# Optimization experiments

Measured on AMD Instinct MI355X. Metric: run time of the kernel, lower is better.

The kernel has to match this reference:

```python
import jax, jax.numpy as jnp
import numpy as np

IMG = 2048
STRIDES = [8, 16, 32, 64, 128]
A = 9                       # num_cell_anchors
CLASS_NUM = 16              # num_classes - 1
TOPK = 1000                 # config.test_layer_topk
MAX_DELTA = float(np.log(1000.0 / 16.0))

_LEVEL_N = [(IMG // s) * (IMG // s) * A for s in STRIDES]


def setup_inputs() -> dict:
    key = jax.random.key(0)
    inp = {}
    for l, n in enumerate(_LEVEL_N):
        key, k1, k2, k3, k4 = jax.random.split(key, 5)
        cxcy = jax.random.uniform(k1, (n, 2), minval=0.0, maxval=float(IMG))
        wh = jax.random.uniform(k2, (n, 2), minval=8.0, maxval=128.0)
        inp[f"anchors{l}"] = jnp.concatenate([cxcy - 0.5 * wh, cxcy + 0.5 * wh], axis=1)
        # logits biased negative like a trained RetinaNet cls head (prior_prob init)
        inp[f"cls{l}"] = jax.random.normal(k3, (1, n, CLASS_NUM), dtype=jnp.float32) - 4.0
        inp[f"reg{l}"] = jax.random.normal(k4, (1, n, 8), dtype=jnp.float32) * 0.1
    return inp


def bbox_transform_inv(rois, deltas):
    # standard box decode (restore_bbox with unnormalize=False)
    w = rois[:, 2] - rois[:, 0]
    h = rois[:, 3] - rois[:, 1]
    cx = rois[:, 0] + 0.5 * w
    cy = rois[:, 1] + 0.5 * h
    pcx = cx + deltas[:, 0] * w
    pcy = cy + deltas[:, 1] * h
    pw = w * jnp.exp(jnp.minimum(deltas[:, 2], MAX_DELTA))
    ph = h * jnp.exp(jnp.minimum(deltas[:, 3], MAX_DELTA))
    return jnp.stack([pcx - 0.5 * pw, pcy - 0.5 * ph,
                      pcx + 0.5 * pw, pcy + 0.5 * ph], axis=1)


def _per_layer(anchors, pred_cls, pred_reg):
    a = anchors.reshape(-1, 4)
    c = pred_cls[0].reshape(-1, CLASS_NUM)
    r = pred_reg[0].reshape(-1, 8)[:, :4]
    if a.shape[0] > TOPK:
        ruler = jnp.max(c, axis=1)                  # max score over classes
        _, inds = jax.lax.top_k(ruler, TOPK)        # irregular topk + gather
        a = jnp.take(a, inds, axis=0)
        c = jnp.take(c, inds, axis=0)
        r = jnp.take(r, inds, axis=0)
    return a, jax.nn.sigmoid(c), r


def reference(anchors0, cls0, reg0, anchors1, cls1, reg1, anchors2, cls2, reg2,
              anchors3, cls3, reg3, anchors4, cls4, reg4):
    levels = [(anchors0, cls0, reg0), (anchors1, cls1, reg1),
              (anchors2, cls2, reg2), (anchors3, cls3, reg3),
              (anchors4, cls4, reg4)]
    kept = [_per_layer(a, c, r) for a, c, r in levels]
    keep_anchors = jnp.concatenate([k[0] for k in kept], axis=0)   # [K,4]
    keep_cls = jnp.concatenate([k[1] for k in kept], axis=0)       # [K,C]
    keep_reg = jnp.concatenate([k[2] for k in kept], axis=0)       # [K,4]
    K = keep_cls.shape[0]
    tag = jnp.tile(jnp.arange(CLASS_NUM, dtype=keep_cls.dtype) + 1.0, (K,)).reshape(-1, 1)
    pred_scores = keep_cls.reshape(-1, 1)                          # [K*C,1]
    pred_bbox = bbox_transform_inv(keep_anchors, keep_reg)         # [K,4]
    pred_bbox = jnp.tile(pred_bbox, (1, CLASS_NUM)).reshape(-1, 4) # [K*C,4]
    return jnp.concatenate([pred_bbox, pred_scores, tag], axis=1)  # [K*C,6]
```

## Files before the change

kernel.cpp:

```cpp
#include <hip/hip_runtime.h>
#include <math.h>

#define NLEV 5
#define TOPKK 1000
#define NCLS 16
#define NPART 16
#define HP 4
#define PART_CAP 256
#define CAND_TOT 2048
#define NCHUNK 3069u
#define CPB 6u
#define NB 512u
#define HISTSZ (NLEV * 256)

__device__ __forceinline__ int lev_of_chunk(unsigned c) {
    if (c < 2304u) return 0;
    if (c < 2880u) return 1;
    if (c < 3024u) return 2;
    if (c < 3060u) return 3;
    return 4;
}
__device__ __forceinline__ unsigned lev_base(int l) {
    unsigned b = 0u;
    if (l == 1) b = 589824u;
    if (l == 2) b = 737280u;
    if (l == 3) b = 774144u;
    if (l == 4) b = 783360u;
    return b;
}

struct Ptrs {
    const float* anc[NLEV];
    const float* cls[NLEV];
    const float* reg[NLEV];
};

__device__ __forceinline__ unsigned f2key(float f) {
    unsigned u = __float_as_uint(f);
    return (u & 0x80000000u) ? ~u : (u | 0x80000000u);
}

__device__ __forceinline__ float max4(float4 v) {
    return fmaxf(fmaxf(v.x, v.y), fmaxf(v.z, v.w));
}

__device__ __forceinline__ void arrive_wait(unsigned* base, bool dowait) {
    __syncthreads();
    if (threadIdx.x == 0) {
        __builtin_amdgcn_fence(__ATOMIC_RELEASE, "agent");
        unsigned g = blockIdx.x & 15u;
        unsigned a = __hip_atomic_fetch_add(base + g * 16u, 1u,
                        __ATOMIC_RELAXED, __HIP_MEMORY_SCOPE_AGENT);
        if (a == NB / 16u - 1u) {
            unsigned m = __hip_atomic_fetch_add(base + 256u, 1u,
                            __ATOMIC_RELAXED, __HIP_MEMORY_SCOPE_AGENT);
            if (m == 15u) {
                #pragma unroll
                for (unsigned r = 0; r < 16u; r++)
                    __hip_atomic_store(base + 512u + r * 16u, 1u,
                                       __ATOMIC_RELAXED, __HIP_MEMORY_SCOPE_AGENT);
            }
        }
        if (dowait) {
            while (!__hip_atomic_load(base + 512u + g * 16u,
                        __ATOMIC_RELAXED, __HIP_MEMORY_SCOPE_AGENT))
                __builtin_amdgcn_s_sleep(4);
            __builtin_amdgcn_fence(__ATOMIC_ACQUIRE, "agent");
        }
    }
    __syncthreads();
}

__device__ __forceinline__ void sel256(unsigned c, unsigned rem,
                                       unsigned* wsum, unsigned* aux) {
    int t = threadIdx.x, lane = t & 63, wv = t >> 6;
    unsigned s = c;
    #pragma unroll
    for (int d = 1; d < 64; d <<= 1) {
        unsigned o = __shfl_down(s, d, 64);
        if (lane + d < 64) s += o;
    }
    if (lane == 0) wsum[wv] = s;
    __syncthreads();
    unsigned incl = s;
    #pragma unroll
    for (int w2 = 1; w2 < 4; w2++) if (wv + w2 < 4) incl += wsum[wv + w2];
    unsigned above = incl - c;
    if (above < rem && rem <= incl) {
        aux[0] = (unsigned)t;
        aux[1] = rem - above;
    }
    __syncthreads();
}

__global__ __launch_bounds__(256, 2) void k_fused(Ptrs p, unsigned* histA,
        unsigned* histB, unsigned* cnt, unsigned* bar,
        unsigned long long* cand, float* out) {
    __shared__ unsigned long long lbuf[CAND_TOT];
    __shared__ unsigned hh[256];
    __shared__ unsigned wsum[4];
    __shared__ unsigned aux[33];

    const unsigned b = blockIdx.x;
    const int t = threadIdx.x;
    const unsigned c0 = b * CPB;
    const int lev = lev_of_chunk(c0);
    const unsigned ebase = lev_base(lev);

    unsigned keys[CPB];
    hh[t] = 0u;
    __syncthreads();
    #pragma unroll
    for (unsigned j = 0; j < CPB; j++) {
        unsigned ch = c0 + j;
        unsigned k = 0u;
        if (ch < NCHUNK) {
            unsigned loc = ch * 256u + (unsigned)t - ebase;
            const float4* cp = (const float4*)(p.cls[lev]) + (size_t)loc * 4;
            float4 v0 = cp[0], v1 = cp[1], v2 = cp[2], v3 = cp[3];
            float m = fmaxf(fmaxf(max4(v0), max4(v1)), fmaxf(max4(v2), max4(v3)));
            k = f2key(m);
            atomicAdd(&hh[k >> 24], 1u);
        }
        keys[j] = k;
    }
    __syncthreads();
    {
        unsigned v = hh[t];
        if (v) atomicAdd(&histA[(b & (HP - 1u)) * HISTSZ
                                + (unsigned)lev * 256u + (unsigned)t], v);
    }
    arrive_wait(bar, true);

    unsigned cA = 0;
    #pragma unroll
    for (int pp = 0; pp < HP; pp++) cA += histA[pp * HISTSZ + lev * 256 + t];
    sel256(cA, TOPKK, wsum, aux);
    unsigned binA = aux[0], remA = aux[1];
    __syncthreads();

    hh[t] = 0u;
    __syncthreads();
    #pragma unroll
    for (unsigned j = 0; j < CPB; j++) {
        unsigned k = keys[j];
        if ((c0 + j) < NCHUNK && (k >> 24) == binA)
            atomicAdd(&hh[(k >> 16) & 0xFFu], 1u);
    }
    __syncthreads();
    {
        unsigned v = hh[t];
        if (v) atomicAdd(&histB[(b & (HP - 1u)) * HISTSZ
                                + (unsigned)lev * 256u + (unsigned)t], v);
    }
    arrive_wait(bar + 1024, true);

    unsigned cB = 0;
    #pragma unroll
    for (int pp = 0; pp < HP; pp++) cB += histB[pp * HISTSZ + lev * 256 + t];
    sel256(cB, remA, wsum, aux);
    unsigned thresh = (binA << 24) | (aux[0] << 16);
    __syncthreads();

    #pragma unroll
    for (unsigned j = 0; j < CPB; j++) {
        unsigned ch = c0 + j;
        unsigned k = keys[j];
        if (ch < NCHUNK && k >= thresh) {
            unsigned loc = ch * 256u + (unsigned)t - ebase;
            unsigned part = ch & (NPART - 1u);
            unsigned slot = atomicAdd(&cnt[lev * NPART + part], 1u);
            if (slot < PART_CAP)
                cand[((size_t)(lev * NPART + part)) * PART_CAP + slot] =
                    ((unsigned long long)k << 32) | (unsigned)(~loc);
        }
    }

    bool ranker = b < (unsigned)(NLEV * 8);
    arrive_wait(bar + 2048, ranker);
    if (!ranker) return;

    const float MAXD = 4.135166556742356f;
    int l = (int)(b >> 3);
    unsigned sl = b & 7u;

    if (t < NPART) {
        unsigned cc = cnt[l * NPART + t];
        aux[t] = (cc > PART_CAP) ? PART_CAP : cc;
    }
    __syncthreads();
    if (t == 0) {
        unsigned o = 0;
        for (int pp = 0; pp < NPART; pp++) { aux[16 + pp] = o; o += aux[pp]; }
        aux[32] = (o > CAND_TOT) ? CAND_TOT : o;
    }
    __syncthreads();
    unsigned n = aux[32];
    for (int pp = 0; pp < NPART; pp++) {
        unsigned cc = aux[pp], o = aux[16 + pp];
        for (unsigned e = (unsigned)t; e < cc; e += 256u) {
            unsigned dst = o + e;
            if (dst < CAND_TOT)
                lbuf[dst] = cand[((size_t)(l * NPART + pp)) * PART_CAP + e];
        }
    }
    __syncthreads();

    unsigned j = sl * 256u + (unsigned)t;
    if (j >= n) return;
    unsigned long long my = lbuf[j];
    unsigned rank = 0;
    #pragma unroll 8
    for (unsigned q = 0; q < n; q++) rank += (lbuf[q] > my) ? 1u : 0u;
    if (rank >= TOPKK) return;

    unsigned idx = ~((unsigned)(my & 0xFFFFFFFFull));
    float4 an = ((const float4*)p.anc[l])[idx];
    float4 dd = ((const float4*)p.reg[l])[(size_t)idx * 2];
    float w = an.z - an.x, h = an.w - an.y;
    float cx = an.x + 0.5f * w, cy = an.y + 0.5f * h;
    float pcx = cx + dd.x * w, pcy = cy + dd.y * h;
    float pw = w * expf(fminf(dd.z, MAXD));
    float ph = h * expf(fminf(dd.w, MAXD));
    float bx = pcx - 0.5f * pw, by = pcy - 0.5f * ph;
    float bz = pcx + 0.5f * pw, bw = pcy + 0.5f * ph;

    const float4* cp = (const float4*)(p.cls[l]) + (size_t)idx * 4;
    float sg[16];
    #pragma unroll
    for (int g = 0; g < 4; g++) {
        float4 v = cp[g];
        sg[4 * g + 0] = 1.0f / (1.0f + expf(-v.x));
        sg[4 * g + 1] = 1.0f / (1.0f + expf(-v.y));
        sg[4 * g + 2] = 1.0f / (1.0f + expf(-v.z));
        sg[4 * g + 3] = 1.0f / (1.0f + expf(-v.w));
    }
    float4* q = (float4*)(out + (size_t)(l * TOPKK + rank) * (NCLS * 6));
    #pragma unroll
    for (int g = 0; g < 8; g++) {
        float ta = (float)(2 * g + 1), tb = (float)(2 * g + 2);
        q[3 * g + 0] = make_float4(bx, by, bz, bw);
        q[3 * g + 1] = make_float4(sg[2 * g], ta, bx, by);
        q[3 * g + 2] = make_float4(bz, bw, sg[2 * g + 1], tb);
    }
}

extern "C" void kernel_launch(void* const* d_in, const int* in_sizes, int n_in,
                              void* d_out, int out_size, void* d_ws, size_t ws_size,
                              hipStream_t stream) {
    (void)in_sizes; (void)n_in; (void)out_size; (void)ws_size;
    Ptrs p;
    for (int l = 0; l < NLEV; l++) {
        p.anc[l] = (const float*)d_in[3 * l + 0];
        p.cls[l] = (const float*)d_in[3 * l + 1];
        p.reg[l] = (const float*)d_in[3 * l + 2];
    }

    char* w = (char*)d_ws;
    unsigned* histA = (unsigned*)w;
    unsigned* histB = (unsigned*)(w + 20480);
    unsigned* cnt   = (unsigned*)(w + 40960);
    unsigned* bar   = (unsigned*)(w + 41280);
    unsigned long long* cand = (unsigned long long*)(w + 53568);
    float* out = (float*)d_out;

    (void)hipMemsetAsync(w, 0, 53568, stream);
    k_fused<<<dim3(NB), dim3(256), 0, stream>>>(p, histA, histB, cnt, bar,
                                                cand, out);
}
```

Before: 202.0 us.

## Replace counter grid barrier with flag-array monitor barrier and spread atomic contention

The grid barrier changes from hierarchical atomic counters to per-block arrival flags. Block 0 polls all 512 flags with its 256 threads and then releases 16 go-flags. Global histogram atomics are spread over 16 partitions instead of 4, and the candidate partition counters are padded onto separate cache lines, both to cut atomic contention. In exchange the workspace memset grows, the post-barrier histogram reads go from 4 to 16 partitions, and all blocks must wait on block 0 polling serially.

```diff
diff --git a/kernel.cpp b/kernel.cpp
--- a/kernel.cpp
+++ b/kernel.cpp
@@ -5,13 +5,14 @@
 #define TOPKK 1000
 #define NCLS 16
 #define NPART 16
-#define HP 4
+#define HP 16u
 #define PART_CAP 256
 #define CAND_TOT 2048
 #define NCHUNK 3069u
 #define CPB 6u
 #define NB 512u
 #define HISTSZ (NLEV * 256)
+#define BAR_STRIDE 1024u
 
 __device__ __forceinline__ int lev_of_chunk(unsigned c) {
     if (c < 2304u) return 0;
@@ -44,29 +45,51 @@
     return fmaxf(fmaxf(v.x, v.y), fmaxf(v.z, v.w));
 }
 
-__device__ __forceinline__ void arrive_wait(unsigned* base, bool dowait) {
-    __syncthreads();
+__device__ __forceinline__ void bar_arrive(unsigned* inst) {
     if (threadIdx.x == 0) {
         __builtin_amdgcn_fence(__ATOMIC_RELEASE, "agent");
-        unsigned g = blockIdx.x & 15u;
-        unsigned a = __hip_atomic_fetch_add(base + g * 16u, 1u,
+        __hip_atomic_store(inst + blockIdx.x, 1u, __ATOMIC_RELAXED,
+                           __HIP_MEMORY_SCOPE_AGENT);
+    }
+}
+
+__device__ __forceinline__ void bar_monitor_fanout(unsigned* inst, unsigned* wsh) {
+    for (;;) {
+        unsigned f0 = __hip_atomic_load(inst + (unsigned)threadIdx.x,
                         __ATOMIC_RELAXED, __HIP_MEMORY_SCOPE_AGENT);
-        if (a == NB / 16u - 1u) {
-            unsigned m = __hip_atomic_fetch_add(base + 256u, 1u,
-                            __ATOMIC_RELAXED, __HIP_MEMORY_SCOPE_AGENT);
-            if (m == 15u) {
-                #pragma unroll
-                for (unsigned r = 0; r < 16u; r++)
-                    __hip_atomic_store(base + 512u + r * 16u, 1u,
-                                       __ATOMIC_RELAXED, __HIP_MEMORY_SCOPE_AGENT);
-            }
-        }
-        if (dowait) {
-            while (!__hip_atomic_load(base + 512u + g * 16u,
-                        __ATOMIC_RELAXED, __HIP_MEMORY_SCOPE_AGENT))
-                __builtin_amdgcn_s_sleep(4);
+        unsigned f1 = __hip_atomic_load(inst + 256u + (unsigned)threadIdx.x,
+                        __ATOMIC_RELAXED, __HIP_MEMORY_SCOPE_AGENT);
+        unsigned long long bal = __ballot(f0 != 0u && f1 != 0u);
+        if ((threadIdx.x & 63) == 0)
+            wsh[threadIdx.x >> 6] = (bal == 0xFFFFFFFFFFFFFFFFull) ? 1u : 0u;
+        __syncthreads();
+        bool done = wsh[0] && wsh[1] && wsh[2] && wsh[3];
+        __syncthreads();
+        if (done) break;
+        __builtin_amdgcn_s_sleep(2);
+    }
+    if (threadIdx.x < 16)
+        __hip_atomic_store(inst + 768u + (unsigned)threadIdx.x * 16u, 1u,
+                           __ATOMIC_RELAXED, __HIP_MEMORY_SCOPE_AGENT);
+}
+
+__device__ __forceinline__ void bar_waitgo(unsigned* inst) {
+    unsigned g = blockIdx.x & 15u;
+    while (!__hip_atomic_load(inst + 768u + g * 16u, __ATOMIC_RELAXED,
+                              __HIP_MEMORY_SCOPE_AGENT))
+        __builtin_amdgcn_s_sleep(4);
+    __builtin_amdgcn_fence(__ATOMIC_ACQUIRE, "agent");
+}
+
+__device__ __forceinline__ void gridbar(unsigned* inst, unsigned* wsh) {
+    __syncthreads();
+    bar_arrive(inst);
+    if (blockIdx.x == 0) {
+        bar_monitor_fanout(inst, wsh);
+        if (threadIdx.x == 0)
             __builtin_amdgcn_fence(__ATOMIC_ACQUIRE, "agent");
-        }
+    } else if (threadIdx.x == 0) {
+        bar_waitgo(inst);
     }
     __syncthreads();
 }
@@ -99,6 +122,7 @@
     __shared__ unsigned long long lbuf[CAND_TOT];
     __shared__ unsigned hh[256];
     __shared__ unsigned wsum[4];
+    __shared__ unsigned wsh[4];
     __shared__ unsigned aux[33];
 
     const unsigned b = blockIdx.x;
@@ -106,10 +130,11 @@
     const unsigned c0 = b * CPB;
     const int lev = lev_of_chunk(c0);
     const unsigned ebase = lev_base(lev);
+    unsigned* bar0 = bar;
+    unsigned* bar1 = bar + BAR_STRIDE;
+    unsigned* bar2 = bar + 2u * BAR_STRIDE;
 
     unsigned keys[CPB];
-    hh[t] = 0u;
-    __syncthreads();
     #pragma unroll
     for (unsigned j = 0; j < CPB; j++) {
         unsigned ch = c0 + j;
@@ -120,21 +145,25 @@
             float4 v0 = cp[0], v1 = cp[1], v2 = cp[2], v3 = cp[3];
             float m = fmaxf(fmaxf(max4(v0), max4(v1)), fmaxf(max4(v2), max4(v3)));
             k = f2key(m);
-            atomicAdd(&hh[k >> 24], 1u);
         }
         keys[j] = k;
     }
+    hh[t] = 0u;
+    __syncthreads();
+    #pragma unroll
+    for (unsigned j = 0; j < CPB; j++)
+        if (c0 + j < NCHUNK) atomicAdd(&hh[keys[j] >> 24], 1u);
     __syncthreads();
     {
         unsigned v = hh[t];
         if (v) atomicAdd(&histA[(b & (HP - 1u)) * HISTSZ
                                 + (unsigned)lev * 256u + (unsigned)t], v);
     }
-    arrive_wait(bar, true);
+    gridbar(bar0, wsh);
 
     unsigned cA = 0;
     #pragma unroll
-    for (int pp = 0; pp < HP; pp++) cA += histA[pp * HISTSZ + lev * 256 + t];
+    for (unsigned pp = 0; pp < HP; pp++) cA += histA[pp * HISTSZ + lev * 256 + t];
     sel256(cA, TOPKK, wsum, aux);
     unsigned binA = aux[0], remA = aux[1];
     __syncthreads();
@@ -153,11 +182,11 @@
         if (v) atomicAdd(&histB[(b & (HP - 1u)) * HISTSZ
                                 + (unsigned)lev * 256u + (unsigned)t], v);
     }
-    arrive_wait(bar + 1024, true);
+    gridbar(bar1, wsh);
 
     unsigned cB = 0;
     #pragma unroll
-    for (int pp = 0; pp < HP; pp++) cB += histB[pp * HISTSZ + lev * 256 + t];
+    for (unsigned pp = 0; pp < HP; pp++) cB += histB[pp * HISTSZ + lev * 256 + t];
     sel256(cB, remA, wsum, aux);
     unsigned thresh = (binA << 24) | (aux[0] << 16);
     __syncthreads();
@@ -169,7 +198,7 @@
         if (ch < NCHUNK && k >= thresh) {
             unsigned loc = ch * 256u + (unsigned)t - ebase;
             unsigned part = ch & (NPART - 1u);
-            unsigned slot = atomicAdd(&cnt[lev * NPART + part], 1u);
+            unsigned slot = atomicAdd(&cnt[(lev * NPART + part) * 16u], 1u);
             if (slot < PART_CAP)
                 cand[((size_t)(lev * NPART + part)) * PART_CAP + slot] =
                     ((unsigned long long)k << 32) | (unsigned)(~loc);
@@ -177,15 +206,24 @@
     }
 
     bool ranker = b < (unsigned)(NLEV * 8);
-    arrive_wait(bar + 2048, ranker);
-    if (!ranker) return;
+    __syncthreads();
+    bar_arrive(bar2);
+    if (b == 0) {
+        bar_monitor_fanout(bar2, wsh);
+        if (t == 0) __builtin_amdgcn_fence(__ATOMIC_ACQUIRE, "agent");
+    } else if (ranker) {
+        if (t == 0) bar_waitgo(bar2);
+    } else {
+        return;
+    }
+    __syncthreads();
 
     const float MAXD = 4.135166556742356f;
     int l = (int)(b >> 3);
     unsigned sl = b & 7u;
 
     if (t < NPART) {
-        unsigned cc = cnt[l * NPART + t];
+        unsigned cc = cnt[(l * NPART + t) * 16u];
         aux[t] = (cc > PART_CAP) ? PART_CAP : cc;
     }
     __syncthreads();
@@ -258,13 +296,13 @@
 
     char* w = (char*)d_ws;
     unsigned* histA = (unsigned*)w;
-    unsigned* histB = (unsigned*)(w + 20480);
-    unsigned* cnt   = (unsigned*)(w + 40960);
-    unsigned* bar   = (unsigned*)(w + 41280);
-    unsigned long long* cand = (unsigned long long*)(w + 53568);
+    unsigned* histB = (unsigned*)(w + 81920);
+    unsigned* cnt   = (unsigned*)(w + 163840);
+    unsigned* bar   = (unsigned*)(w + 168960);
+    unsigned long long* cand = (unsigned long long*)(w + 181248);
     float* out = (float*)d_out;
 
-    (void)hipMemsetAsync(w, 0, 53568, stream);
+    (void)hipMemsetAsync(w, 0, 181248, stream);
     k_fused<<<dim3(NB), dim3(256), 0, stream>>>(p, histA, histB, cnt, bar,
                                                 cand, out);
 }
```

New measurement: 192.7 us. 1.05x faster.
